# Optimization experiments

Hardware: AMD Instinct MI355X
Metric: run time of the kernel (lower is better)

## Reference

```python
import jax, jax.numpy as jnp
import numpy as np

DIM = 1024
HEADS = 16
DIM_HEAD = 64
WINDOW = 256  # sliding window size == block size
NEG = -1e9


def rms_norm(x, gamma, size):
    # F.normalize(x, dim=-1) * sqrt(size) * gamma
    nrm = jnp.sqrt(jnp.sum(x * x, axis=-1, keepdims=True))
    return x / jnp.maximum(nrm, 1e-12) * (size ** 0.5) * gamma


def sliding_window_attention(q, k, v, window):
    # q,k,v: [b, h, S, d]; causal local attention: key j valid iff i-window <= j <= i
    b, h, S, d = q.shape
    Bk = window
    nb = S // Bk
    qb = q.reshape(b, h, nb, Bk, d)
    kb = k.reshape(b, h, nb, Bk, d)
    vb = v.reshape(b, h, nb, Bk, d)
    # previous key/value block (zeros for block 0; masked out below)
    k_prev = jnp.pad(kb, ((0, 0), (0, 0), (1, 0), (0, 0), (0, 0)))[:, :, :nb]
    v_prev = jnp.pad(vb, ((0, 0), (0, 0), (1, 0), (0, 0), (0, 0)))[:, :, :nb]
    kctx = jnp.concatenate([k_prev, kb], axis=3)  # [b,h,nb,2Bk,d]
    vctx = jnp.concatenate([v_prev, vb], axis=3)
    scale = 1.0 / jnp.sqrt(jnp.asarray(d, q.dtype))
    scores = jnp.einsum('bhnqd,bhnkd->bhnqk', qb, kctx) * scale  # [b,h,nb,Bk,2Bk]
    qi = jnp.arange(Bk)[:, None]          # local query index
    kj = jnp.arange(2 * Bk)[None, :]      # local key index (offset -Bk rel to block start)
    diff = Bk + qi - kj                   # global i - j
    base = (diff >= 0) & (diff <= window)  # [Bk, 2Bk]
    blk = jnp.arange(nb)[:, None, None]
    key_exists = ((blk - 1) * Bk + kj[None]) >= 0  # [nb,1,2Bk] -> broadcast
    mask = base[None] & key_exists                 # [nb,Bk,2Bk]
    scores = jnp.where(mask[None, None], scores, NEG)
    attn = jax.nn.softmax(scores, axis=-1)
    out = jnp.einsum('bhnqk,bhnkd->bhnqd', attn, vctx)
    return out.reshape(b, h, S, d)


def setup_inputs() -> dict:
    key = jax.random.key(0)
    ks = jax.random.split(key, 6)
    b, S = 2, 4096
    dim_inner = HEADS * DIM_HEAD
    x = jax.random.normal(ks[0], (b, S, DIM), dtype=jnp.float32)
    gamma = jnp.ones((DIM,), dtype=jnp.float32)
    W_qkv = jax.random.normal(ks[1], (DIM, 3 * dim_inner), dtype=jnp.float32) * 0.02
    W_gates = jax.random.normal(ks[2], (DIM, HEADS), dtype=jnp.float32) * 0.02
    b_gates = jnp.zeros((HEADS,), dtype=jnp.float32)
    W_out = jax.random.normal(ks[3], (dim_inner, DIM), dtype=jnp.float32) * 0.02
    return {"x": x, "gamma": gamma, "W_qkv": W_qkv, "W_gates": W_gates,
            "b_gates": b_gates, "W_out": W_out}


def reference(x, gamma, W_qkv, W_gates, b_gates, W_out):
    b, S, dim = x.shape
    xn = rms_norm(x, gamma, dim)
    qkv = xn @ W_qkv                                    # [b,S,3*h*d]
    qkv = qkv.reshape(b, S, 3, HEADS, DIM_HEAD)
    q, k, v = [jnp.transpose(t, (0, 2, 1, 3)) for t in
               (qkv[:, :, 0], qkv[:, :, 1], qkv[:, :, 2])]  # [b,h,S,d]
    out = sliding_window_attention(q, k, v, WINDOW)      # [b,h,S,d]
    gates = xn @ W_gates + b_gates                       # [b,S,h]
    out = out * jax.nn.sigmoid(jnp.transpose(gates, (0, 2, 1)))[..., None]
    out = jnp.transpose(out, (0, 2, 1, 3)).reshape(b, S, HEADS * DIM_HEAD)
    return out @ W_out
```

## Files before the change

kernel.cpp:

```cpp
#include <hip/hip_runtime.h>
#include <hip/hip_bf16.h>
#include <stdint.h>

typedef __bf16 bf16;
typedef __bf16 bf16x4 __attribute__((ext_vector_type(4)));
typedef __bf16 bf16x8 __attribute__((ext_vector_type(8)));
typedef float f32x4 __attribute__((ext_vector_type(4)));

#define GLOBAL_AS __attribute__((address_space(1)))
#define LDS_AS __attribute__((address_space(3)))

__device__ __forceinline__ void g2lds16(const bf16* g, bf16* l) {
  __builtin_amdgcn_global_load_lds((const GLOBAL_AS void*)g, (LDS_AS void*)l, 16, 0, 0);
}

__global__ __launch_bounds__(256) void rmsnorm_kernel(
    const float* __restrict__ x, const float* __restrict__ gamma,
    bf16* __restrict__ xn) {
  __shared__ float wss[4];
  const int t = threadIdx.x;
  const size_t row = blockIdx.x;
  const float* xr = x + row * 1024;

  float4 xv = *(const float4*)&xr[t * 4];
  float v[4] = {xv.x, xv.y, xv.z, xv.w};
  float ss = v[0]*v[0] + v[1]*v[1] + v[2]*v[2] + v[3]*v[3];
#pragma unroll
  for (int mm = 1; mm < 64; mm <<= 1) ss += __shfl_xor(ss, mm);
  if ((t & 63) == 0) wss[t >> 6] = ss;
  __syncthreads();
  ss = wss[0] + wss[1] + wss[2] + wss[3];
  float inv = 32.0f / sqrtf(fmaxf(ss, 1e-24f));

  float4 gv = *(const float4*)&gamma[t * 4];
  float gvv[4] = {gv.x, gv.y, gv.z, gv.w};
  bf16x4 outv;
#pragma unroll
  for (int i = 0; i < 4; ++i) outv[i] = (bf16)(v[i] * inv * gvv[i]);
  *(bf16x4*)&xn[row * 1024 + t * 4] = outv;
}

__global__ void transpose_f32_bf16(const float* __restrict__ in, bf16* __restrict__ out,
                                   int R, int C) {
  __shared__ bf16 tile[32][33];
  const int tx = threadIdx.x, ty = threadIdx.y;
  const int c0 = blockIdx.x * 32, r0 = blockIdx.y * 32;
#pragma unroll
  for (int i = 0; i < 32; i += 8)
    tile[ty + i][tx] = (bf16)in[(size_t)(r0 + ty + i) * C + c0 + tx];
  __syncthreads();
#pragma unroll
  for (int i = 0; i < 32; i += 8)
    out[(size_t)(c0 + ty + i) * R + r0 + tx] = tile[tx][ty + i];
}

__global__ __launch_bounds__(256) void wg_transpose(const float* __restrict__ Wg,
                                                    bf16* __restrict__ BtAug) {
  int idx = blockIdx.x * 256 + threadIdx.x;
  int n = idx >> 10, k = idx & 1023;
  BtAug[(size_t)(3072 + n) * 1024 + k] = (bf16)Wg[(size_t)k * 16 + n];
}

template <typename OutT>
__global__ __launch_bounds__(256) void gemm_bt_128(
    const bf16* __restrict__ A, const bf16* __restrict__ Bt,
    OutT* __restrict__ C, int M, int N, int K) {
  __shared__ bf16 lA[128 * 64];
  __shared__ bf16 lB[128 * 64];
  const int t = threadIdx.x;
  const int w = t >> 6, lane = t & 63;
  const int col0 = lane & 15, quad = lane >> 4;
  const int m0 = blockIdx.y * 128, n0 = blockIdx.x * 128;
  const int wr = (w >> 1) * 64, wc = (w & 1) * 64;

  const int lrow = t >> 3;
  const int sswz = (((t & 7) ^ (lrow & 7)) << 3);

  f32x4 acc[4][4] = {};

  for (int k0 = 0; k0 < K; k0 += 64) {
    __syncthreads();
#pragma unroll
    for (int c = 0; c < 4; ++c) {
      g2lds16(A  + (size_t)(m0 + c * 32 + lrow) * K + k0 + sswz, &lA[c * 2048 + w * 512]);
      g2lds16(Bt + (size_t)(n0 + c * 32 + lrow) * K + k0 + sswz, &lB[c * 2048 + w * 512]);
    }
    __syncthreads();

#pragma unroll
    for (int kh = 0; kh < 2; ++kh) {
      bf16x8 af[4], bfr[4];
#pragma unroll
      for (int i = 0; i < 4; ++i) {
        int row = wr + i * 16 + col0;
        af[i] = *(const bf16x8*)&lA[row * 64 + (((kh * 4 + quad) ^ (row & 7)) << 3)];
      }
#pragma unroll
      for (int j = 0; j < 4; ++j) {
        int row = wc + j * 16 + col0;
        bfr[j] = *(const bf16x8*)&lB[row * 64 + (((kh * 4 + quad) ^ (row & 7)) << 3)];
      }
#pragma unroll
      for (int i = 0; i < 4; ++i)
#pragma unroll
        for (int j = 0; j < 4; ++j)
          acc[i][j] = __builtin_amdgcn_mfma_f32_16x16x32_bf16(af[i], bfr[j], acc[i][j], 0, 0, 0);
    }
  }

#pragma unroll
  for (int i = 0; i < 4; ++i)
#pragma unroll
    for (int j = 0; j < 4; ++j)
#pragma unroll
      for (int r = 0; r < 4; ++r) {
        int row = m0 + wr + i * 16 + quad * 4 + r;
        int col = n0 + wc + j * 16 + col0;
        C[(size_t)row * N + col] = (OutT)acc[i][j][r];
      }
}

template <typename OutT>
__global__ __launch_bounds__(512, 2) void gemm_bt_256(
    const bf16* __restrict__ A, const bf16* __restrict__ Bt,
    OutT* __restrict__ C, int M, int N, int K) {
  extern __shared__ bf16 lds[];
  bf16* A0 = lds;
  bf16* B0 = lds + 16384;
  bf16* A1 = lds + 32768;
  bf16* B1 = lds + 49152;

  const int t = threadIdx.x;
  const int w = t >> 6, lane = t & 63;
  const int wm = w >> 2, wn = w & 3;
  const int col0 = lane & 15, quad = lane >> 4;
  const int s_sub = lane >> 3;
  const int sswz = (((lane & 7) ^ s_sub) << 3);

  int nwg = gridDim.x * gridDim.y;
  int bid = blockIdx.y * gridDim.x + blockIdx.x;
  int swz = bid;
  if ((nwg & 7) == 0) swz = (bid & 7) * (nwg >> 3) + (bid >> 3);
  const int n0 = (swz % gridDim.x) * 256;
  const int m0 = (swz / gridDim.x) * 256;

  const bf16* Abase = A + (size_t)m0 * (size_t)K;

  auto stageA = [&](int ks, int c, bf16* dstA) {
    int rb = (w < 4) ? (c * 32 + w * 8) : (128 + c * 32 + (w - 4) * 8);
    g2lds16(Abase + (size_t)(rb + s_sub) * K + ks + sswz, dstA + rb * 64);
  };
  auto stageB = [&](int ks, int c, bf16* dstB) {
    int rb = c * 64 + w * 8;
    int gr = n0 + rb + s_sub;
    gr = (gr < N) ? gr : (N - 1);
    g2lds16(Bt + (size_t)gr * (size_t)K + ks + sswz, dstB + rb * 64);
  };

  f32x4 acc[8][4] = {};
  const int NT = K >> 6;
  const int NI = NT >> 1;

#pragma unroll
  for (int c = 0; c < 4; ++c) stageA(0, c, A0);
#pragma unroll
  for (int c = 0; c < 4; ++c) stageB(0, c, B0);
#pragma unroll
  for (int c = 0; c < 3; ++c) stageA(64, c, A1);
  asm volatile("s_waitcnt vmcnt(3)" ::: "memory");
  __builtin_amdgcn_s_barrier();

  for (int i = 0; i < NI; ++i) {
#pragma unroll
    for (int h = 0; h < 2; ++h) {
      bf16* cA  = h ? A1 : A0;
      bf16* cB  = h ? B1 : B0;
      bf16* sA0 = h ? A0 : A1;
      bf16* sB0 = h ? B0 : B1;
      bf16* sA1 = h ? A1 : A0;
      int t0 = 2 * i + 1 + h;
      int t1 = 2 * i + 2 + h;
      int k0 = ((t0 < NT) ? t0 : 0) << 6;
      int k1 = ((t1 < NT) ? t1 : 0) << 6;
#pragma unroll
      for (int q = 0; q < 4; ++q) {
        bf16x8 af[2][2], bv[4][2];
#pragma unroll
        for (int m2 = 0; m2 < 2; ++m2) {
          int ar = wm * 128 + (q * 2 + m2) * 16 + col0;
#pragma unroll
          for (int ks = 0; ks < 2; ++ks)
            af[m2][ks] = *(const bf16x8*)&cA[ar * 64 + (((ks * 4 + quad) ^ (ar & 7)) << 3)];
        }
#pragma unroll
        for (int nj = 0; nj < 4; ++nj) {
          int br = wn * 64 + nj * 16 + col0;
#pragma unroll
          for (int ks = 0; ks < 2; ++ks)
            bv[nj][ks] = *(const bf16x8*)&cB[br * 64 + (((ks * 4 + quad) ^ (br & 7)) << 3)];
        }
        if (q == 0) {
          stageA(k0, 3, sA0);
          stageB(k0, 0, sB0); stageB(k0, 1, sB0);
          stageB(k0, 2, sB0); stageB(k0, 3, sB0);
        } else {
          stageA(k1, q - 1, sA1);
        }
        __builtin_amdgcn_s_barrier();
        asm volatile("s_waitcnt lgkmcnt(0)" ::: "memory");
        __builtin_amdgcn_s_setprio(1);
#pragma unroll
        for (int ks = 0; ks < 2; ++ks)
#pragma unroll
          for (int m2 = 0; m2 < 2; ++m2)
#pragma unroll
            for (int nj = 0; nj < 4; ++nj)
              acc[q * 2 + m2][nj] = __builtin_amdgcn_mfma_f32_16x16x32_bf16(
                  af[m2][ks], bv[nj][ks], acc[q * 2 + m2][nj], 0, 0, 0);
        __builtin_amdgcn_s_setprio(0);
        if (q == 3) asm volatile("s_waitcnt vmcnt(3)" ::: "memory");
        __builtin_amdgcn_s_barrier();
      }
    }
  }
  asm volatile("s_waitcnt vmcnt(0)" ::: "memory");

#pragma unroll
  for (int mi = 0; mi < 8; ++mi)
#pragma unroll
    for (int nj = 0; nj < 4; ++nj) {
      int col = n0 + wn * 64 + nj * 16 + col0;
      if (col < N) {
        size_t base = (size_t)(m0 + wm * 128 + mi * 16 + quad * 4) * N + col;
#pragma unroll
        for (int r = 0; r < 4; ++r)
          C[base + (size_t)r * N] = (OutT)acc[mi][nj][r];
      }
    }
}

#define NEG_BIG -1e30f
__global__ __launch_bounds__(256) void attn_kernel(
    const bf16* __restrict__ qkv, const float* __restrict__ bg,
    bf16* __restrict__ attnO) {
  __shared__ bf16 lQ[64 * 64];
  __shared__ bf16 lKV[320 * 64];
  __shared__ bf16 lP[4 * 16 * 32];

  const int t = threadIdx.x;
  const int w = t >> 6, lane = t & 63;
  const int col0 = lane & 15, quad = lane >> 4;

  const int blk = blockIdx.x;
  const int g = blk & 63;
  const int h = (blk >> 6) & 15;
  const int bb = blk >> 10;
  const int qs = g * 64;

  const size_t rs = 3200;
  const bf16* qbase = qkv + ((size_t)bb * 4096) * rs + h * 64;

  for (int c = t; c < 64 * 8; c += 256) {
    int row = c >> 3, ck = c & 7;
    *(uint4*)&lQ[row * 64 + ((ck ^ (row & 7)) << 3)] =
        *(const uint4*)(qbase + (size_t)(qs + row) * rs + ck * 8);
  }
  for (int c = t; c < 320 * 8; c += 256) {
    int row = c >> 3, ck = c & 7;
    int j = qs - 256 + row;
    uint4 val = {0, 0, 0, 0};
    if (j >= 0) val = *(const uint4*)(qbase + 1024 + (size_t)j * rs + ck * 8);
    *(uint4*)&lKV[row * 64 + ((ck ^ (row & 7)) << 3)] = val;
  }
  __syncthreads();

  const int qrow = w * 16 + col0;
  bf16x8 a0 = *(const bf16x8*)&lQ[qrow * 64 + ((quad ^ (qrow & 7)) << 3)];
  bf16x8 a1 = *(const bf16x8*)&lQ[qrow * 64 + (((4 + quad) ^ (qrow & 7)) << 3)];
  f32x4 s[20];
#pragma unroll
  for (int kt = 0; kt < 20; ++kt) {
    int krow = kt * 16 + col0;
    bf16x8 b0 = *(const bf16x8*)&lKV[krow * 64 + ((quad ^ (krow & 7)) << 3)];
    bf16x8 b1 = *(const bf16x8*)&lKV[krow * 64 + (((4 + quad) ^ (krow & 7)) << 3)];
    f32x4 z = {};
    z = __builtin_amdgcn_mfma_f32_16x16x32_bf16(a0, b0, z, 0, 0, 0);
    z = __builtin_amdgcn_mfma_f32_16x16x32_bf16(a1, b1, z, 0, 0, 0);
    s[kt] = z;
  }
  __syncthreads();

  {
    const int jl = t & 31, dg = t >> 5;
#pragma unroll
    for (int cc = 0; cc < 10; ++cc) {
      int j = qs - 256 + cc * 32 + jl;
      bf16 tmp[8];
      if (j >= 0) {
        *(uint4*)tmp = *(const uint4*)(qbase + 2048 + (size_t)j * rs + dg * 8);
      } else {
#pragma unroll
        for (int d2 = 0; d2 < 8; ++d2) tmp[d2] = (bf16)0.f;
      }
      int ck = cc * 4 + (jl >> 3);
      int wi = jl & 7;
#pragma unroll
      for (int d2 = 0; d2 < 8; ++d2) {
        int d = dg * 8 + d2;
        lKV[d * 320 + ((ck ^ (d & 7)) << 3) + wi] = tmp[d2];
      }
    }
  }

  float mrow[4] = {NEG_BIG, NEG_BIG, NEG_BIG, NEG_BIG};
  float lrow[4] = {0, 0, 0, 0};
#pragma unroll
  for (int kt = 0; kt < 20; ++kt) {
    int c = kt * 16 + col0;
#pragma unroll
    for (int r = 0; r < 4; ++r) {
      int ql = w * 16 + quad * 4 + r;
      bool valid = (c >= ql) && (c <= ql + 256) && (qs - 256 + c >= 0);
      float sv = valid ? s[kt][r] * 0.125f : NEG_BIG;
      s[kt][r] = sv;
      mrow[r] = fmaxf(mrow[r], sv);
    }
  }
#pragma unroll
  for (int mm = 1; mm < 16; mm <<= 1)
#pragma unroll
    for (int r = 0; r < 4; ++r) mrow[r] = fmaxf(mrow[r], __shfl_xor(mrow[r], mm));
#pragma unroll
  for (int kt = 0; kt < 20; ++kt)
#pragma unroll
    for (int r = 0; r < 4; ++r) {
      float p = __expf(s[kt][r] - mrow[r]);
      s[kt][r] = p;
      lrow[r] += p;
    }
#pragma unroll
  for (int mm = 1; mm < 16; mm <<= 1)
#pragma unroll
    for (int r = 0; r < 4; ++r) lrow[r] += __shfl_xor(lrow[r], mm);

  __syncthreads();

  f32x4 o[4] = {};
  bf16* pw = &lP[w * 512];
#pragma unroll
  for (int kc = 0; kc < 10; ++kc) {
#pragma unroll
    for (int r = 0; r < 4; ++r) {
      pw[(quad * 4 + r) * 32 + col0]      = (bf16)s[2 * kc][r];
      pw[(quad * 4 + r) * 32 + 16 + col0] = (bf16)s[2 * kc + 1][r];
    }
    asm volatile("s_waitcnt lgkmcnt(0)" ::: "memory");
    bf16x8 pa = *(const bf16x8*)&pw[col0 * 32 + quad * 8];
#pragma unroll
    for (int n = 0; n < 4; ++n) {
      int d = n * 16 + col0;
      bf16x8 bvv = *(const bf16x8*)&lKV[d * 320 + (((kc * 4 + quad) ^ (d & 7)) << 3)];
      o[n] = __builtin_amdgcn_mfma_f32_16x16x32_bf16(pa, bvv, o[n], 0, 0, 0);
    }
  }

  const bf16* gbase = qkv + ((size_t)bb * 4096) * rs + 3072 + h;
  const float bgh = bg[h];
#pragma unroll
  for (int r = 0; r < 4; ++r) {
    int ql = w * 16 + quad * 4 + r;
    int srow = qs + ql;
    float logit = (float)gbase[(size_t)srow * rs] + bgh;
    float gate = 1.f / (1.f + __expf(-logit));
    float scale = gate / lrow[r];
#pragma unroll
    for (int n = 0; n < 4; ++n)
      attnO[((size_t)bb * 4096 + srow) * 1024 + h * 64 + n * 16 + col0] =
          (bf16)(o[n][r] * scale);
  }
}

extern "C" void kernel_launch(void* const* d_in, const int* in_sizes, int n_in,
                              void* d_out, int out_size, void* d_ws, size_t ws_size,
                              hipStream_t stream) {
  const float *x = nullptr, *gamma = nullptr, *Wqkv = nullptr,
              *Wg = nullptr, *bg = nullptr, *Wout = nullptr;
  for (int i = 0; i < n_in; ++i) {
    switch (in_sizes[i]) {
      case 8388608: x     = (const float*)d_in[i]; break;
      case 1024:    gamma = (const float*)d_in[i]; break;
      case 3145728: Wqkv  = (const float*)d_in[i]; break;
      case 16384:   Wg    = (const float*)d_in[i]; break;
      case 16:      bg    = (const float*)d_in[i]; break;
      case 1048576: Wout  = (const float*)d_in[i]; break;
    }
  }
  float* out = (float*)d_out;

  static bool attr_done = false;
  if (!attr_done) {
    hipFuncSetAttribute(reinterpret_cast<const void*>(&gemm_bt_256<bf16>),
                        hipFuncAttributeMaxDynamicSharedMemorySize, 131072);
    attr_done = true;
  }

  char* ws = (char*)d_ws;
  bf16* qkv   = (bf16*)ws;  ws += (size_t)8192 * 3200 * 2;
  bf16* xn    = (bf16*)ws;
  bf16* attnO = (bf16*)ws;  ws += (size_t)8192 * 1024 * 2;
  bf16* BtAug = (bf16*)ws;  ws += (size_t)3200 * 1024 * 2;
  bf16* WoutT = (bf16*)ws;  ws += (size_t)1024 * 1024 * 2;

  hipMemsetAsync(BtAug + (size_t)3088 * 1024, 0, (size_t)112 * 1024 * 2, stream);

  rmsnorm_kernel<<<8192, 256, 0, stream>>>(x, gamma, xn);
  transpose_f32_bf16<<<dim3(3072 / 32, 1024 / 32), dim3(32, 8), 0, stream>>>(Wqkv, BtAug, 1024, 3072);
  wg_transpose<<<64, 256, 0, stream>>>(Wg, BtAug);
  transpose_f32_bf16<<<dim3(1024 / 32, 1024 / 32), dim3(32, 8), 0, stream>>>(Wout, WoutT, 1024, 1024);
  gemm_bt_256<bf16><<<dim3(13, 32), 512, 131072, stream>>>(xn, BtAug, qkv, 8192, 3200, 1024);
  attn_kernel<<<2048, 256, 0, stream>>>(qkv, bg, attnO);
  gemm_bt_128<float><<<dim3(1024 / 128, 8192 / 128), 256, 0, stream>>>(attnO, WoutT, out, 8192, 1024, 1024);
}
```

Before: 265.1 us.

## Load B fragments once per K-tile and restage GEMM prefetch schedule

The GEMM main loop now reads each K-tile's B fragments from LDS once and reuses them across all four M sub-steps, where before they were re-read every sub-step. The global-to-LDS prefetch is reordered so B for the next tile is staged first and A is spread over later sub-steps, with new vmcnt wait thresholds. This cuts LDS read traffic and changes how loads overlap with MFMA work. In exchange, bv stays live across the whole tile and raises register pressure, and the hand-tuned vmcnt counts must exactly match the new issue order or the kernel will race.

```diff
diff --git a/kernel.cpp b/kernel.cpp
--- a/kernel.cpp
+++ b/kernel.cpp
@@ -162,50 +162,40 @@
   const int NI = NT >> 1;
 
 #pragma unroll
-  for (int c = 0; c < 4; ++c) stageA(0, c, A0);
-#pragma unroll
   for (int c = 0; c < 4; ++c) stageB(0, c, B0);
-#pragma unroll
-  for (int c = 0; c < 3; ++c) stageA(64, c, A1);
+  stageA(0, 0, A0);
+  stageA(0, 1, A0); stageA(0, 2, A0); stageA(0, 3, A0);
   asm volatile("s_waitcnt vmcnt(3)" ::: "memory");
   __builtin_amdgcn_s_barrier();
 
   for (int i = 0; i < NI; ++i) {
 #pragma unroll
     for (int h = 0; h < 2; ++h) {
-      bf16* cA  = h ? A1 : A0;
-      bf16* cB  = h ? B1 : B0;
-      bf16* sA0 = h ? A0 : A1;
-      bf16* sB0 = h ? B0 : B1;
-      bf16* sA1 = h ? A1 : A0;
-      int t0 = 2 * i + 1 + h;
-      int t1 = 2 * i + 2 + h;
-      int k0 = ((t0 < NT) ? t0 : 0) << 6;
-      int k1 = ((t1 < NT) ? t1 : 0) << 6;
-#pragma unroll
-      for (int q = 0; q < 4; ++q) {
-        bf16x8 af[2][2], bv[4][2];
+      bf16* cA = h ? A1 : A0;
+      bf16* cB = h ? B1 : B0;
+      bf16* nA = h ? A0 : A1;
+      bf16* nB = h ? B0 : B1;
+      int tn = 2 * i + h + 1;
+      int kn = ((tn < NT) ? tn : 0) << 6;
+
+      bf16x8 bv[4][2];
+#pragma unroll
+      for (int nj = 0; nj < 4; ++nj) {
+        int br = wn * 64 + nj * 16 + col0;
+#pragma unroll
+        for (int ks = 0; ks < 2; ++ks)
+          bv[nj][ks] = *(const bf16x8*)&cB[br * 64 + (((ks * 4 + quad) ^ (br & 7)) << 3)];
+      }
+      {
+        bf16x8 af[2][2];
 #pragma unroll
         for (int m2 = 0; m2 < 2; ++m2) {
-          int ar = wm * 128 + (q * 2 + m2) * 16 + col0;
+          int ar = wm * 128 + m2 * 16 + col0;
 #pragma unroll
           for (int ks = 0; ks < 2; ++ks)
             af[m2][ks] = *(const bf16x8*)&cA[ar * 64 + (((ks * 4 + quad) ^ (ar & 7)) << 3)];
         }
-#pragma unroll
-        for (int nj = 0; nj < 4; ++nj) {
-          int br = wn * 64 + nj * 16 + col0;
-#pragma unroll
-          for (int ks = 0; ks < 2; ++ks)
-            bv[nj][ks] = *(const bf16x8*)&cB[br * 64 + (((ks * 4 + quad) ^ (br & 7)) << 3)];
-        }
-        if (q == 0) {
-          stageA(k0, 3, sA0);
-          stageB(k0, 0, sB0); stageB(k0, 1, sB0);
-          stageB(k0, 2, sB0); stageB(k0, 3, sB0);
-        } else {
-          stageA(k1, q - 1, sA1);
-        }
+        stageB(kn, 0, nB); stageB(kn, 1, nB);
         __builtin_amdgcn_s_barrier();
         asm volatile("s_waitcnt lgkmcnt(0)" ::: "memory");
         __builtin_amdgcn_s_setprio(1);
@@ -215,10 +205,41 @@
           for (int m2 = 0; m2 < 2; ++m2)
 #pragma unroll
             for (int nj = 0; nj < 4; ++nj)
-              acc[q * 2 + m2][nj] = __builtin_amdgcn_mfma_f32_16x16x32_bf16(
-                  af[m2][ks], bv[nj][ks], acc[q * 2 + m2][nj], 0, 0, 0);
+              acc[m2][nj] = __builtin_amdgcn_mfma_f32_16x16x32_bf16(
+                  af[m2][ks], bv[nj][ks], acc[m2][nj], 0, 0, 0);
         __builtin_amdgcn_s_setprio(0);
-        if (q == 3) asm volatile("s_waitcnt vmcnt(3)" ::: "memory");
+        asm volatile("s_waitcnt vmcnt(4)" ::: "memory");
+        __builtin_amdgcn_s_barrier();
+      }
+
+#pragma unroll
+      for (int p = 1; p < 4; ++p) {
+        bf16x8 af[2][2];
+#pragma unroll
+        for (int m2 = 0; m2 < 2; ++m2) {
+          int ar = wm * 128 + (p * 2 + m2) * 16 + col0;
+#pragma unroll
+          for (int ks = 0; ks < 2; ++ks)
+            af[m2][ks] = *(const bf16x8*)&cA[ar * 64 + (((ks * 4 + quad) ^ (ar & 7)) << 3)];
+        }
+        if (p == 1)      { stageB(kn, 2, nB); stageB(kn, 3, nB); stageA(kn, 0, nA); }
+        else if (p == 2) { stageA(kn, 1, nA); stageA(kn, 2, nA); }
+        else             { stageA(kn, 3, nA); }
+        __builtin_amdgcn_s_barrier();
+        asm volatile("s_waitcnt lgkmcnt(0)" ::: "memory");
+        __builtin_amdgcn_s_setprio(1);
+#pragma unroll
+        for (int ks = 0; ks < 2; ++ks)
+#pragma unroll
+          for (int m2 = 0; m2 < 2; ++m2)
+#pragma unroll
+            for (int nj = 0; nj < 4; ++nj)
+              acc[p * 2 + m2][nj] = __builtin_amdgcn_mfma_f32_16x16x32_bf16(
+                  af[m2][ks], bv[nj][ks], acc[p * 2 + m2][nj], 0, 0, 0);
+        __builtin_amdgcn_s_setprio(0);
+        if (p == 1)      asm volatile("s_waitcnt vmcnt(6)" ::: "memory");
+        else if (p == 2) asm volatile("s_waitcnt vmcnt(7)" ::: "memory");
+        else             asm volatile("s_waitcnt vmcnt(3)" ::: "memory");
         __builtin_amdgcn_s_barrier();
       }
     }
```

Measured after the change: 256.7 us. 3.1% less time.
